# Performance work log

Hardware: AMD Instinct MI355X
Metric: run time of the kernel (lower is better)

Reference implementation:

```python
import jax, jax.numpy as jnp
import numpy as np

N_NODES = 50000
N_EDGES = 800000
N_GRAPHS = 256
F_IN = 112   # num_features
DIM = 32     # hidden dim of 2nd GIN layer
OUT_DIM = 64 # output_dim
BN_EPS = 1e-5


def setup_inputs() -> dict:
    key = jax.random.key(0)
    ks = jax.random.split(key, 20)
    def w(k, shape, s=0.05):
        return jax.random.normal(k, shape, dtype=jnp.float32) * s
    return {
        "x": jax.random.normal(ks[0], (N_NODES, F_IN), dtype=jnp.float32),
        "src": jax.random.randint(ks[1], (N_EDGES,), 0, N_NODES),
        "dst": jax.random.randint(ks[2], (N_EDGES,), 0, N_NODES),
        "batch": jnp.sort(jax.random.randint(ks[3], (N_NODES,), 0, N_GRAPHS)),
        # GIN layer 1 MLP: Linear(112,112) -> ReLU -> Linear(112,112)
        "g1_w1": w(ks[4], (F_IN, F_IN)), "g1_b1": jnp.zeros((F_IN,), jnp.float32),
        "g1_w2": w(ks[5], (F_IN, F_IN)), "g1_b2": jnp.zeros((F_IN,), jnp.float32),
        "bn1_g": jnp.ones((F_IN,), jnp.float32), "bn1_b": jnp.zeros((F_IN,), jnp.float32),
        # GIN layer 2 MLP: Linear(112,32) -> ReLU -> Linear(32,32)
        "g2_w1": w(ks[6], (F_IN, DIM)), "g2_b1": jnp.zeros((DIM,), jnp.float32),
        "g2_w2": w(ks[7], (DIM, DIM)), "g2_b2": jnp.zeros((DIM,), jnp.float32),
        "bn2_g": jnp.ones((DIM,), jnp.float32), "bn2_b": jnp.zeros((DIM,), jnp.float32),
        # graph-level head
        "fcxd_w": w(ks[8], (DIM, OUT_DIM)), "fcxd_b": jnp.zeros((OUT_DIM,), jnp.float32),
        "fc1_w": w(ks[9], (64, 32)), "fc1_b": jnp.zeros((32,), jnp.float32),
        "fc2_w": w(ks[10], (32, 16)), "fc2_b": jnp.zeros((16,), jnp.float32),
        "fc3_w": w(ks[11], (16, 8)), "fc3_b": jnp.zeros((8,), jnp.float32),
        "fc4_w": w(ks[12], (8, 2)), "fc4_b": jnp.zeros((2,), jnp.float32),
        "fc5_w": w(ks[13], (2, 1)), "fc5_b": jnp.zeros((1,), jnp.float32),
    }


def _batchnorm(h, g, b):
    # training-mode BatchNorm1d: batch statistics over node axis
    m = h.mean(axis=0)
    v = h.var(axis=0)
    return (h - m) * jax.lax.rsqrt(v + BN_EPS) * g + b


def reference(x, src, dst, batch,
              g1_w1, g1_b1, g1_w2, g1_b2, bn1_g, bn1_b,
              g2_w1, g2_b1, g2_w2, g2_b2, bn2_g, bn2_b,
              fcxd_w, fcxd_b, fc1_w, fc1_b, fc2_w, fc2_b,
              fc3_w, fc3_b, fc4_w, fc4_b, fc5_w, fc5_b):
    # --- GIN layer 1: agg = sum_{j in N(i)} x_j ; h = MLP(x + agg) (eps=0) ---
    agg = jax.ops.segment_sum(x[src], dst, num_segments=N_NODES)
    h = x + agg
    h = jnp.maximum(h @ g1_w1 + g1_b1, 0.0) @ g1_w2 + g1_b2
    h = jnp.maximum(h, 0.0)                     # F.relu after conv
    h = _batchnorm(h, bn1_g, bn1_b)
    # --- GIN layer 2 ---
    agg = jax.ops.segment_sum(h[src], dst, num_segments=N_NODES)
    h = h + agg
    h = jnp.maximum(h @ g2_w1 + g2_b1, 0.0) @ g2_w2 + g2_b2
    h = jnp.maximum(h, 0.0)
    h = _batchnorm(h, bn2_g, bn2_b)
    # --- global_add_pool over graph ids ---
    pooled = jax.ops.segment_sum(h, batch, num_segments=N_GRAPHS)  # [G, 32]
    z = jnp.maximum(pooled @ fcxd_w + fcxd_b, 0.0)  # dropout = identity (eval)
    # dense head: NO activations between fc1..fc5 in the original code
    z = z @ fc1_w + fc1_b
    z = z @ fc2_w + fc2_b
    z = z @ fc3_w + fc3_b
    z = z @ fc4_w + fc4_b
    z = z @ fc5_w + fc5_b
    return z  # [N_GRAPHS, 1]
```

## Files before the change

### kernel.cpp

```cpp
#include <hip/hip_runtime.h>
#include <hip/hip_fp16.h>

#define N_NODES 50000
#define N_GRAPHS 256
#define N_EDGES 800000
#define F_IN 112
#define DIM 32
#define BN_EPS 1e-5
#define HROW 128
#define CAP 64
#define CB 391
#define CBCAP 2560
#define CHUNK 8192
#define NPART 98
#define GEMM_MB 782
#define WS 40
#define SENT2 0xC350C350u

typedef __attribute__((ext_vector_type(8))) _Float16 half8;
typedef __attribute__((ext_vector_type(4))) float float4v;

__device__ inline unsigned short f2h_u(float f) {
    union { __half h; unsigned short u; } v; v.h = __float2half(f); return v.u;
}
__device__ inline float h2f_u(unsigned short u) {
    union { unsigned short u; __half h; } v; v.u = u; return __half2float(v.h);
}

__device__ inline void acc8(const uint4& u, float* ax) {
    const __half2* h = (const __half2*)&u;
#pragma unroll
    for (int p = 0; p < 4; p++) {
        float2 f = __half22float2(h[p]);
        ax[2 * p] += f.x;
        ax[2 * p + 1] += f.y;
    }
}

__device__ inline void w_split_body(const float* __restrict__ W, int K, int N, int Kpad,
                                    unsigned short* __restrict__ hi_t,
                                    unsigned short* __restrict__ lo_t, int idx) {
    if (idx >= N * Kpad) return;
    int n = idx / Kpad, k = idx - n * Kpad;
    float v = (k < K) ? W[(size_t)k * N + n] : 0.f;
    unsigned short h = f2h_u(v);
    hi_t[idx] = h;
    lo_t[idx] = f2h_u(v - h2f_u(h));
}

#define MB_P  NPART
#define MB_XH (MB_P + 3126)
#define MB_W1 (MB_XH + 14)
#define MB_W2 (MB_W1 + 14)
#define MB_W4 (MB_W2 + 1)
#define MB_GB (MB_W4 + 49)
__global__ __launch_bounds__(1024) void build_kernel(
        const int* __restrict__ src, const int* __restrict__ dst,
        int* __restrict__ gcur,
        int* __restrict__ bucket,
        const float* __restrict__ X, __half* __restrict__ Xh,
        const float* __restrict__ g1_w1, unsigned short* w1h, unsigned short* w1l,
        const float* __restrict__ g1_w2, unsigned short* w2h, unsigned short* w2l,
        const float* __restrict__ g2_w2, unsigned short* w4h, unsigned short* w4l,
        const int* __restrict__ batch, int* __restrict__ goff) {
    int b = blockIdx.x;
    int t = threadIdx.x;
    if (b < MB_P) {
        __shared__ int hist[512];
        __shared__ int lofs[512];
        __shared__ int lcur[512];
        __shared__ int gbase[512];
        __shared__ int staging[CHUNK];
        int base = b * CHUNK;
        int total = min(CHUNK, N_EDGES - base);
        for (int i = t; i < 512; i += 1024) hist[i] = 0;
        __syncthreads();
        int d[8], s[8];
#pragma unroll
        for (int j = 0; j < 8; j++) {
            int i = base + j * 1024 + t;
            if (i < N_EDGES) {
                d[j] = __builtin_nontemporal_load(dst + i);
                s[j] = __builtin_nontemporal_load(src + i);
            } else {
                d[j] = -1;
            }
        }
#pragma unroll
        for (int j = 0; j < 8; j++) {
            if (d[j] >= 0) atomicAdd(&hist[d[j] >> 7], 1);
        }
        __syncthreads();
        if (t < 512) lofs[t] = hist[t];
        __syncthreads();
        for (int o = 1; o < 512; o <<= 1) {
            int add = (t < 512 && t >= o) ? lofs[t - o] : 0;
            __syncthreads();
            if (t < 512) lofs[t] += add;
            __syncthreads();
        }
        if (t < CB) {
            gbase[t] = (hist[t] > 0) ? atomicAdd(&gcur[t], hist[t]) : 0;
        }
        if (t < 512) lcur[t] = lofs[t] - hist[t];
        __syncthreads();
#pragma unroll
        for (int j = 0; j < 8; j++) {
            if (d[j] >= 0) {
                int bb = d[j] >> 7;
                int p = atomicAdd(&lcur[bb], 1);
                staging[p] = (d[j] << 16) | s[j];
            }
        }
        __syncthreads();
        for (int p = t; p < total; p += 1024) {
            int e = staging[p];
            int bb = ((unsigned)e >> 16) >> 7;
            int ls = lofs[bb] - hist[bb];
            int di = gbase[bb] + (p - ls);
            if (di < CBCAP) bucket[(size_t)bb * CBCAP + di] = e;
        }
    } else if (b < MB_XH) {
        int idx = (b - MB_P) * 1024 + t;
        if (idx >= (N_NODES + 1) * (HROW / 2)) return;
        int row = idx >> 6, c2 = idx & 63;
        int col = c2 * 2;
        float2 v = make_float2(0.f, 0.f);
        if (row < N_NODES && col < F_IN) v = *(const float2*)(X + (size_t)row * F_IN + col);
        ((__half2*)Xh)[idx] = __floats2half2_rn(v.x, v.y);
    } else if (b < MB_W1) {
        w_split_body(g1_w1, F_IN, F_IN, 128, w1h, w1l, (b - MB_XH) * 1024 + t);
    } else if (b < MB_W2) {
        w_split_body(g1_w2, F_IN, F_IN, 128, w2h, w2l, (b - MB_W1) * 1024 + t);
    } else if (b < MB_W4) {
        w_split_body(g2_w2, DIM, DIM, 32, w4h, w4l, (b - MB_W2) * 1024 + t);
    } else {
        int i = (b - MB_W4) * 1024 + t;
        if (i >= N_NODES) return;
        int cur = batch[i];
        int prev = (i == 0) ? -1 : batch[i - 1];
        for (int g = prev + 1; g <= cur; g++) goff[g] = i;
        if (i == N_NODES - 1) {
            for (int g = cur + 1; g <= N_GRAPHS; g++) goff[g] = N_NODES;
        }
    }
}

__global__ __launch_bounds__(1024, 8) void gin1_fused(const float* __restrict__ X,
        const __half* __restrict__ Xh,
        const int* __restrict__ gcur,
        const int* __restrict__ bucket,
        const unsigned short* __restrict__ W1h, const unsigned short* __restrict__ W1l,
        const float* __restrict__ b1,
        const unsigned short* __restrict__ W2h, const unsigned short* __restrict__ W2l,
        const float* __restrict__ b2,
        __half* __restrict__ Ch, float* __restrict__ pbuf, int M) {
    constexpr int N = 112, Kpad = 128, TS = 136, AS = 136;
    __shared__ __align__(16) unsigned short Afull[64 * AS];
    __shared__ __align__(16) unsigned short T1[64 * TS];
    __shared__ __align__(16) unsigned short Wh[N * WS];
    __shared__ __align__(16) unsigned short Wl[N * WS];
    __shared__ __align__(16) unsigned short bins[64][CAP];
    __shared__ int lcur[64];
    float* sls = (float*)Afull;
    int t = threadIdx.x;
    int lane = t & 63, wid = t >> 6;
    int r0 = blockIdx.x * 64;
    int m = lane & 15, quad = lane >> 4;
    int rg = wid & 3, ng = wid >> 2;
    int nt0 = ng, nt1 = ng + 4;
    bool has1 = (nt1 < 7);

    for (int i = t; i < 64 * CAP / 2; i += 1024) ((unsigned int*)bins)[i] = SENT2;
    if (t < 64) lcur[t] = 0;

    for (int idx = t; idx < N * 8; idx += 1024) {
        int n = idx >> 3, w = idx & 7;
        int gsrc = n * (Kpad / 4) + w;
        ((uint2*)&Wh[n * WS])[w] = ((const uint2*)W1h)[gsrc];
        ((uint2*)&Wl[n * WS])[w] = ((const uint2*)W1l)[gsrc];
    }
    __syncthreads();

    {
        int cb = blockIdx.x >> 1, half = blockIdx.x & 1;
        int count = min(gcur[cb], CBCAP);
        for (int i = t; i < count; i += 1024) {
            int e = bucket[(size_t)cb * CBCAP + i];
            int l = ((unsigned)e >> 16) & 127;
            if ((l >> 6) == half) {
                int c = atomicAdd(&lcur[l & 63], 1);
                if (c < CAP) bins[l & 63][c] = (unsigned short)(e & 0xFFFF);
            }
        }
    }
    __syncthreads();

    int fl = lane & 15, eg = lane >> 4;
#pragma unroll 1
    for (int i = 0; i < 4; i++) {
        int row = wid * 4 + i;
        int grow = r0 + row;
        int deg = min(lcur[row], CAP);
        float ax[8] = {0.f, 0.f, 0.f, 0.f, 0.f, 0.f, 0.f, 0.f};
        const unsigned short* pl = bins[row];
        int nb = (deg + 3) >> 2;
#pragma unroll 1
        for (int b = 0; b < nb; b += 4) {
            int s0 = pl[(b + 0) * 4 + eg];
            int s1 = pl[(b + 1) * 4 + eg];
            int s2 = pl[(b + 2) * 4 + eg];
            int s3 = pl[(b + 3) * 4 + eg];
            uint4 u0 = *(const uint4*)(Xh + (size_t)s0 * HROW + fl * 8);
            uint4 u1 = *(const uint4*)(Xh + (size_t)s1 * HROW + fl * 8);
            uint4 u2 = *(const uint4*)(Xh + (size_t)s2 * HROW + fl * 8);
            uint4 u3 = *(const uint4*)(Xh + (size_t)s3 * HROW + fl * 8);
            acc8(u0, ax); acc8(u1, ax); acc8(u2, ax); acc8(u3, ax);
        }
#pragma unroll
        for (int p = 0; p < 8; p++) {
            ax[p] += __shfl_xor(ax[p], 16);
            ax[p] += __shfl_xor(ax[p], 32);
        }
        if (eg == 0) {
            if (grow < M && fl < 14) {
                float4 sa = *(const float4*)(X + (size_t)grow * F_IN + fl * 8);
                float4 sb = *(const float4*)(X + (size_t)grow * F_IN + fl * 8 + 4);
                ax[0] += sa.x; ax[1] += sa.y; ax[2] += sa.z; ax[3] += sa.w;
                ax[4] += sb.x; ax[5] += sb.y; ax[6] += sb.z; ax[7] += sb.w;
            }
            uint4 o;
            __half2* oh = (__half2*)&o;
#pragma unroll
            for (int p = 0; p < 4; p++) oh[p] = __floats2half2_rn(ax[2 * p], ax[2 * p + 1]);
            *(uint4*)&Afull[row * AS + fl * 8] = o;
        }
    }
    {
        int i = t;
        T1[(i >> 4) * TS + 112 + (i & 15)] = 0;
    }

    float4v acc0 = {0.f, 0.f, 0.f, 0.f}, acc1 = {0.f, 0.f, 0.f, 0.f};

    for (int c = 0; c < 4; c++) {
        int kc = c * 32;
        if (c > 0) {
            for (int idx = t; idx < N * 8; idx += 1024) {
                int n = idx >> 3, w = idx & 7;
                int gsrc = n * (Kpad / 4) + (kc >> 2) + w;
                ((uint2*)&Wh[n * WS])[w] = ((const uint2*)W1h)[gsrc];
                ((uint2*)&Wl[n * WS])[w] = ((const uint2*)W1l)[gsrc];
            }
        }
        __syncthreads();
        half8 a = *(const half8*)&Afull[(rg * 16 + m) * AS + kc + quad * 8];
        {
            half8 bh = *(const half8*)&Wh[(nt0 * 16 + m) * WS + quad * 8];
            half8 bl = *(const half8*)&Wl[(nt0 * 16 + m) * WS + quad * 8];
            acc0 = __builtin_amdgcn_mfma_f32_16x16x32_f16(a, bh, acc0, 0, 0, 0);
            acc0 = __builtin_amdgcn_mfma_f32_16x16x32_f16(a, bl, acc0, 0, 0, 0);
        }
        if (has1) {
            half8 bh = *(const half8*)&Wh[(nt1 * 16 + m) * WS + quad * 8];
            half8 bl = *(const half8*)&Wl[(nt1 * 16 + m) * WS + quad * 8];
            acc1 = __builtin_amdgcn_mfma_f32_16x16x32_f16(a, bh, acc1, 0, 0, 0);
            acc1 = __builtin_amdgcn_mfma_f32_16x16x32_f16(a, bl, acc1, 0, 0, 0);
        }
        __syncthreads();
    }

    {
        int col = nt0 * 16 + m;
        float bb = b1[col];
#pragma unroll
        for (int r = 0; r < 4; r++)
            T1[(rg * 16 + quad * 4 + r) * TS + col] = f2h_u(fmaxf(acc0[r] + bb, 0.f));
        acc0 = (float4v){0.f, 0.f, 0.f, 0.f};
    }
    if (has1) {
        int col = nt1 * 16 + m;
        float bb = b1[col];
#pragma unroll
        for (int r = 0; r < 4; r++)
            T1[(rg * 16 + quad * 4 + r) * TS + col] = f2h_u(fmaxf(acc1[r] + bb, 0.f));
        acc1 = (float4v){0.f, 0.f, 0.f, 0.f};
    }
    __syncthreads();

    for (int c = 0; c < 4; c++) {
        int kc = c * 32;
        for (int idx = t; idx < N * 8; idx += 1024) {
            int n = idx >> 3, w = idx & 7;
            int gsrc = n * (Kpad / 4) + (kc >> 2) + w;
            ((uint2*)&Wh[n * WS])[w] = ((const uint2*)W2h)[gsrc];
            ((uint2*)&Wl[n * WS])[w] = ((const uint2*)W2l)[gsrc];
        }
        __syncthreads();
        half8 a = *(const half8*)&T1[(rg * 16 + m) * TS + kc + quad * 8];
        {
            half8 bh = *(const half8*)&Wh[(nt0 * 16 + m) * WS + quad * 8];
            half8 bl = *(const half8*)&Wl[(nt0 * 16 + m) * WS + quad * 8];
            acc0 = __builtin_amdgcn_mfma_f32_16x16x32_f16(a, bh, acc0, 0, 0, 0);
            acc0 = __builtin_amdgcn_mfma_f32_16x16x32_f16(a, bl, acc0, 0, 0, 0);
        }
        if (has1) {
            half8 bh = *(const half8*)&Wh[(nt1 * 16 + m) * WS + quad * 8];
            half8 bl = *(const half8*)&Wl[(nt1 * 16 + m) * WS + quad * 8];
            acc1 = __builtin_amdgcn_mfma_f32_16x16x32_f16(a, bh, acc1, 0, 0, 0);
            acc1 = __builtin_amdgcn_mfma_f32_16x16x32_f16(a, bl, acc1, 0, 0, 0);
        }
        __syncthreads();
    }

    float st_s0 = 0.f, st_q0 = 0.f, st_s1 = 0.f, st_q1 = 0.f;
    {
        int col = nt0 * 16 + m;
        float bb = b2[col];
#pragma unroll
        for (int r = 0; r < 4; r++) {
            int row = r0 + rg * 16 + quad * 4 + r;
            float v = fmaxf(acc0[r] + bb, 0.f);
            if (row < M) {
                Ch[(size_t)row * HROW + col] = __float2half(v);
                st_s0 += v;
                st_q0 += v * v;
            }
        }
    }
    if (has1) {
        int col = nt1 * 16 + m;
        float bb = b2[col];
#pragma unroll
        for (int r = 0; r < 4; r++) {
            int row = r0 + rg * 16 + quad * 4 + r;
            float v = fmaxf(acc1[r] + bb, 0.f);
            if (row < M) {
                Ch[(size_t)row * HROW + col] = __float2half(v);
                st_s1 += v;
                st_q1 += v * v;
            }
        }
    }
    if (t < 128) {
        int row = r0 + (t >> 1), o = (t & 1) * 8;
        if (row < M) *(uint4*)((unsigned short*)Ch + (size_t)row * HROW + 112 + o) = make_uint4(0, 0, 0, 0);
    }
    st_s0 += __shfl_xor(st_s0, 16); st_s0 += __shfl_xor(st_s0, 32);
    st_q0 += __shfl_xor(st_q0, 16); st_q0 += __shfl_xor(st_q0, 32);
    st_s1 += __shfl_xor(st_s1, 16); st_s1 += __shfl_xor(st_s1, 32);
    st_q1 += __shfl_xor(st_q1, 16); st_q1 += __shfl_xor(st_q1, 32);
    if (quad == 0) {
        sls[rg * 2 * N + nt0 * 16 + m] = st_s0;
        sls[rg * 2 * N + N + nt0 * 16 + m] = st_q0;
        if (has1) {
            sls[rg * 2 * N + nt1 * 16 + m] = st_s1;
            sls[rg * 2 * N + N + nt1 * 16 + m] = st_q1;
        }
    }
    __syncthreads();
    if (t < 2 * N) {
        pbuf[(size_t)blockIdx.x * 2 * N + t] = sls[0 * 2 * N + t] + sls[1 * 2 * N + t] +
                                               sls[2 * 2 * N + t] + sls[3 * 2 * N + t];
    }
}

__global__ __launch_bounds__(256) void bn1_w3(const float* __restrict__ pbuf,
                                              const float* __restrict__ gg,
                                              const float* __restrict__ bb,
                                              const float* __restrict__ W,
                                              unsigned short* __restrict__ w3h,
                                              unsigned short* __restrict__ w3l,
                                              float* __restrict__ c0,
                                              __half* __restrict__ ysent, int M) {
    __shared__ double red[256];
    __shared__ float sv[2];
    int j = blockIdx.x;
    int t = threadIdx.x;
    if (j == 0 && t >= 64 && t < 96) ysent[t - 64] = __float2half(0.f);
    double sum = 0.0, sq = 0.0;
    for (int i = t; i < GEMM_MB; i += 256) {
        sum += (double)pbuf[(size_t)i * 2 * F_IN + j];
        sq  += (double)pbuf[(size_t)i * 2 * F_IN + F_IN + j];
    }
    red[t] = sum;
    __syncthreads();
    for (int o = 128; o > 0; o >>= 1) { if (t < o) red[t] += red[t + o]; __syncthreads(); }
    double total_sum = red[0];
    __syncthreads();
    red[t] = sq;
    __syncthreads();
    for (int o = 128; o > 0; o >>= 1) { if (t < o) red[t] += red[t + o]; __syncthreads(); }
    if (t == 0) {
        double mean = total_sum / M;
        double var = red[0] / M - mean * mean;
        double sc = (double)gg[j] / sqrt(var + BN_EPS);
        sv[0] = (float)sc;
        sv[1] = (float)((double)bb[j] - mean * sc);
    }
    __syncthreads();
    if (t < DIM) {
        float w = W[(size_t)j * DIM + t];
        float v = sv[0] * w;
        unsigned short h = f2h_u(v);
        w3h[t * 128 + j] = h;
        w3l[t * 128 + j] = f2h_u(v - h2f_u(h));
        atomicAdd(&c0[t], sv[1] * w);
    }
}

template <int NT, int KC, int ASG, int CHS>
__global__ __launch_bounds__(256) void gemm_mfma_h(const unsigned short* __restrict__ A,
                                                   const unsigned short* __restrict__ Whi,
                                                   const unsigned short* __restrict__ Wlo,
                                                   __half* __restrict__ Ch, int M) {
    constexpr int N = NT * 16;
    constexpr int Kpad = KC * 32;
    __shared__ __align__(16) unsigned short Ah[64 * WS];
    __shared__ __align__(16) unsigned short Wh[N * WS];
    __shared__ __align__(16) unsigned short Wl[N * WS];
    int t = threadIdx.x;
    int lane = t & 63, wid = t >> 6;
    int r0 = blockIdx.x * 64;
    int m = lane & 15, quad = lane >> 4;

    float4v acc[NT];
#pragma unroll
    for (int nt = 0; nt < NT; nt++) acc[nt] = (float4v){0.f, 0.f, 0.f, 0.f};

    for (int c = 0; c < KC; c++) {
        int kc = c * 32;
        {
            int row = t >> 2, seg = t & 3;
            int grow = r0 + row;
            uint4 v = make_uint4(0, 0, 0, 0);
            if (grow < M) v = *(const uint4*)(A + (size_t)grow * ASG + kc + seg * 8);
            *(uint4*)&Ah[row * WS + seg * 8] = v;
        }
        for (int idx = t; idx < N * 8; idx += 256) {
            int n = idx >> 3, w = idx & 7;
            int gsrc = n * (Kpad / 4) + (kc >> 2) + w;
            ((uint2*)&Wh[n * WS])[w] = ((const uint2*)Whi)[gsrc];
            ((uint2*)&Wl[n * WS])[w] = ((const uint2*)Wlo)[gsrc];
        }
        __syncthreads();
        half8 a = *(const half8*)&Ah[(wid * 16 + m) * WS + quad * 8];
#pragma unroll
        for (int nt = 0; nt < NT; nt++) {
            half8 b_h = *(const half8*)&Wh[(nt * 16 + m) * WS + quad * 8];
            half8 b_l = *(const half8*)&Wl[(nt * 16 + m) * WS + quad * 8];
            acc[nt] = __builtin_amdgcn_mfma_f32_16x16x32_f16(a, b_h, acc[nt], 0, 0, 0);
            acc[nt] = __builtin_amdgcn_mfma_f32_16x16x32_f16(a, b_l, acc[nt], 0, 0, 0);
        }
        __syncthreads();
    }
#pragma unroll
    for (int nt = 0; nt < NT; nt++) {
        int col = nt * 16 + m;
#pragma unroll
        for (int r = 0; r < 4; r++) {
            int row = r0 + wid * 16 + quad * 4 + r;
            if (row < M) Ch[(size_t)row * CHS + col] = __float2half(acc[nt][r]);
        }
    }
}

__global__ __launch_bounds__(512, 8) void gin2_fused(const __half* __restrict__ Y,
        const int* __restrict__ gcur,
        const int* __restrict__ bucket,
        const float* __restrict__ c0, const float* __restrict__ cb1,
        const unsigned short* __restrict__ W4h, const unsigned short* __restrict__ W4l,
        const float* __restrict__ bias,
        float* __restrict__ C, float* __restrict__ pbuf, int M) {
    constexpr int N = 32;
    __shared__ __align__(16) unsigned short As[64 * WS];
    __shared__ __align__(16) unsigned short Wh[N * WS];
    __shared__ __align__(16) unsigned short Wl[N * WS];
    __shared__ __align__(16) unsigned short bins[64][CAP];
    __shared__ int lcur[64];
    __shared__ float sls[4][2 * N];
    int t = threadIdx.x;
    int lane = t & 63, wid = t >> 6;
    int r0 = blockIdx.x * 64;
    int m = lane & 15, quad = lane >> 4;
    int rg = wid & 3, nt = wid >> 2;

    for (int i = t; i < 64 * CAP / 2; i += 512) ((unsigned int*)bins)[i] = SENT2;
    if (t < 64) lcur[t] = 0;

    for (int idx = t; idx < N * 8; idx += 512) {
        int n = idx >> 3, w = idx & 7;
        int gsrc = n * 8 + w;
        ((uint2*)&Wh[n * WS])[w] = ((const uint2*)W4h)[gsrc];
        ((uint2*)&Wl[n * WS])[w] = ((const uint2*)W4l)[gsrc];
    }
    __syncthreads();

    {
        int cb = blockIdx.x >> 1, half = blockIdx.x & 1;
        int count = min(gcur[cb], CBCAP);
        for (int i = t; i < count; i += 512) {
            int e = bucket[(size_t)cb * CBCAP + i];
            int l = ((unsigned)e >> 16) & 127;
            if ((l >> 6) == half) {
                int c = atomicAdd(&lcur[l & 63], 1);
                if (c < CAP) bins[l & 63][c] = (unsigned short)(e & 0xFFFF);
            }
        }
    }
    __syncthreads();

    int seg = lane & 3, eg = lane >> 2;
#pragma unroll 1
    for (int i = 0; i < 8; i++) {
        int row = wid * 8 + i;
        int grow = r0 + row;
        int deg = min(lcur[row], CAP);
        float ax[8] = {0.f, 0.f, 0.f, 0.f, 0.f, 0.f, 0.f, 0.f};
        if (grow < M) {
            const unsigned short* pl = bins[row];
            int s[4];
#pragma unroll
            for (int j = 0; j < 4; j++) s[j] = pl[j * 16 + eg];
            uint4 u[4];
#pragma unroll
            for (int j = 0; j < 4; j++) u[j] = *(const uint4*)(Y + (size_t)s[j] * DIM + seg * 8);
#pragma unroll
            for (int j = 0; j < 4; j++) acc8(u[j], ax);
        }
#pragma unroll
        for (int p = 0; p < 8; p++) {
            ax[p] += __shfl_xor(ax[p], 4);
            ax[p] += __shfl_xor(ax[p], 8);
            ax[p] += __shfl_xor(ax[p], 16);
            ax[p] += __shfl_xor(ax[p], 32);
        }
        if (eg == 0) {
            uint4 o = make_uint4(0, 0, 0, 0);
            if (grow < M) {
                uint4 sv = *(const uint4*)(Y + (size_t)grow * DIM + seg * 8);
                float deg1 = (float)(deg + 1);
                const __half2* sh = (const __half2*)&sv;
                __half2* oh = (__half2*)&o;
#pragma unroll
                for (int p = 0; p < 4; p++) {
                    float2 sf = __half22float2(sh[p]);
                    int f0 = seg * 8 + 2 * p;
                    float zx = fmaxf(sf.x + ax[2 * p] + deg1 * c0[f0] + cb1[f0], 0.f);
                    float zy = fmaxf(sf.y + ax[2 * p + 1] + deg1 * c0[f0 + 1] + cb1[f0 + 1], 0.f);
                    oh[p] = __floats2half2_rn(zx, zy);
                }
            }
            *(uint4*)&As[row * WS + seg * 8] = o;
        }
    }
    __syncthreads();

    float4v acc = {0.f, 0.f, 0.f, 0.f};
    half8 a = *(const half8*)&As[(rg * 16 + m) * WS + quad * 8];
    half8 bh = *(const half8*)&Wh[(nt * 16 + m) * WS + quad * 8];
    half8 bl = *(const half8*)&Wl[(nt * 16 + m) * WS + quad * 8];
    acc = __builtin_amdgcn_mfma_f32_16x16x32_f16(a, bh, acc, 0, 0, 0);
    acc = __builtin_amdgcn_mfma_f32_16x16x32_f16(a, bl, acc, 0, 0, 0);

    int col = nt * 16 + m;
    float b = bias[col];
    float s_loc = 0.f, q_loc = 0.f;
#pragma unroll
    for (int r = 0; r < 4; r++) {
        int row = r0 + rg * 16 + quad * 4 + r;
        float v = fmaxf(acc[r] + b, 0.f);
        if (row < M) {
            C[(size_t)row * N + col] = v;
            s_loc += v;
            q_loc += v * v;
        }
    }
    s_loc += __shfl_xor(s_loc, 16); s_loc += __shfl_xor(s_loc, 32);
    q_loc += __shfl_xor(q_loc, 16); q_loc += __shfl_xor(q_loc, 32);
    if (quad == 0) {
        sls[rg][col] = s_loc;
        sls[rg][N + col] = q_loc;
    }
    __syncthreads();
    if (t < 2 * N) {
        pbuf[(size_t)blockIdx.x * 2 * N + t] = sls[0][t] + sls[1][t] + sls[2][t] + sls[3][t];
    }
}

template <int F, int BLOCKS>
__global__ __launch_bounds__(256) void bn_finalize_par(const float* __restrict__ pbuf,
                                                       const float* __restrict__ g,
                                                       const float* __restrict__ b,
                                                       float* __restrict__ s,
                                                       float* __restrict__ tt, int M) {
    __shared__ double red[256];
    int j = blockIdx.x;
    int t = threadIdx.x;
    double sum = 0.0, sq = 0.0;
    for (int i = t; i < BLOCKS; i += 256) {
        sum += (double)pbuf[(size_t)i * 2 * F + j];
        sq  += (double)pbuf[(size_t)i * 2 * F + F + j];
    }
    red[t] = sum;
    __syncthreads();
    for (int o = 128; o > 0; o >>= 1) { if (t < o) red[t] += red[t + o]; __syncthreads(); }
    double total_sum = red[0];
    __syncthreads();
    red[t] = sq;
    __syncthreads();
    for (int o = 128; o > 0; o >>= 1) { if (t < o) red[t] += red[t + o]; __syncthreads(); }
    if (t == 0) {
        double mean = total_sum / M;
        double var = red[0] / M - mean * mean;
        double sc = (double)g[j] / sqrt(var + BN_EPS);
        s[j] = (float)sc;
        tt[j] = (float)((double)b[j] - mean * sc);
    }
}

__global__ __launch_bounds__(256) void pool_head(const float* __restrict__ H2, const int* __restrict__ goff,
                                                 const float* __restrict__ s2, const float* __restrict__ t2,
                                                 const float* __restrict__ fcxd_w, const float* __restrict__ fcxd_b,
                                                 const float* __restrict__ fc1_w, const float* __restrict__ fc1_b,
                                                 const float* __restrict__ fc2_w, const float* __restrict__ fc2_b,
                                                 const float* __restrict__ fc3_w, const float* __restrict__ fc3_b,
                                                 const float* __restrict__ fc4_w, const float* __restrict__ fc4_b,
                                                 const float* __restrict__ fc5_w, const float* __restrict__ fc5_b,
                                                 float* __restrict__ out) {
    __shared__ float red[256];
    __shared__ float p[64];
    __shared__ float z[64];
    int g = blockIdx.x, t = threadIdx.x;
    int r0 = goff[g], r1 = goff[g + 1];
    int cnt = r1 - r0;
    int j = t & 31, rr = t >> 5;
    float a = 0.f;
    for (int r = r0 + rr; r < r1; r += 8) a += H2[(size_t)r * DIM + j];
    red[t] = a;
    __syncthreads();
    if (t < 32) {
        float ssum = 0.f;
        for (int q = 0; q < 8; q++) ssum += red[q * 32 + j];
        p[j] = s2[j] * ssum + (float)cnt * t2[j];
    }
    __syncthreads();
    if (t < 64) {
        float acc = fcxd_b[t];
        for (int i = 0; i < 32; i++) acc += p[i] * fcxd_w[i * 64 + t];
        z[t] = fmaxf(acc, 0.f);
    }
    __syncthreads();
    if (t < 32) {
        float acc = fc1_b[t];
        for (int i = 0; i < 64; i++) acc += z[i] * fc1_w[i * 32 + t];
        p[t] = acc;
    }
    __syncthreads();
    if (t < 16) {
        float acc = fc2_b[t];
        for (int i = 0; i < 32; i++) acc += p[i] * fc2_w[i * 16 + t];
        z[t] = acc;
    }
    __syncthreads();
    if (t < 8) {
        float acc = fc3_b[t];
        for (int i = 0; i < 16; i++) acc += z[i] * fc3_w[i * 8 + t];
        p[t] = acc;
    }
    __syncthreads();
    if (t < 2) {
        float acc = fc4_b[t];
        for (int i = 0; i < 8; i++) acc += p[i] * fc4_w[i * 2 + t];
        z[t] = acc;
    }
    __syncthreads();
    if (t == 0) {
        out[g] = z[0] * fc5_w[0] + z[1] * fc5_w[1] + fc5_b[0];
    }
}

extern "C" void kernel_launch(void* const* d_in, const int* in_sizes, int n_in,
                              void* d_out, int out_size, void* d_ws, size_t ws_size,
                              hipStream_t stream) {
    const float* x     = (const float*)d_in[0];
    const int*   src   = (const int*)d_in[1];
    const int*   dst   = (const int*)d_in[2];
    const int*   batch = (const int*)d_in[3];
    const float* g1_w1 = (const float*)d_in[4];
    const float* g1_b1 = (const float*)d_in[5];
    const float* g1_w2 = (const float*)d_in[6];
    const float* g1_b2 = (const float*)d_in[7];
    const float* bn1_g = (const float*)d_in[8];
    const float* bn1_b = (const float*)d_in[9];
    const float* g2_w1 = (const float*)d_in[10];
    const float* g2_b1 = (const float*)d_in[11];
    const float* g2_w2 = (const float*)d_in[12];
    const float* g2_b2 = (const float*)d_in[13];
    const float* bn2_g = (const float*)d_in[14];
    const float* bn2_b = (const float*)d_in[15];
    const float* fcxd_w = (const float*)d_in[16];
    const float* fcxd_b = (const float*)d_in[17];
    const float* fc1_w = (const float*)d_in[18];
    const float* fc1_b = (const float*)d_in[19];
    const float* fc2_w = (const float*)d_in[20];
    const float* fc2_b = (const float*)d_in[21];
    const float* fc3_w = (const float*)d_in[22];
    const float* fc3_b = (const float*)d_in[23];
    const float* fc4_w = (const float*)d_in[24];
    const float* fc4_b = (const float*)d_in[25];
    const float* fc5_w = (const float*)d_in[26];
    const float* fc5_b = (const float*)d_in[27];
    float* out = (float*)d_out;
    char* ws = (char*)d_ws;

    size_t off = 0;
    auto take = [&](size_t bytes) { size_t o = off; off += (bytes + 255) & ~(size_t)255; return o; };
    int* gcur      = (int*)(ws + take((size_t)CB * 4));
    float* c0      = (float*)(ws + take(DIM * 4));
    unsigned short* w3h = (unsigned short*)(ws + take((size_t)DIM * 128 * 2));
    unsigned short* w3l = (unsigned short*)(ws + take((size_t)DIM * 128 * 2));
    size_t zero_bytes = off;
    int* bucket    = (int*)(ws + take((size_t)CB * CBCAP * 4));
    int* goff      = (int*)(ws + take((size_t)(N_GRAPHS + 4) * 4));
    float* s2      = (float*)(ws + take(DIM * 4));
    float* t2      = (float*)(ws + take(DIM * 4));
    float* pb1     = (float*)(ws + take((size_t)GEMM_MB * 2 * F_IN * 4));
    float* pb2     = (float*)(ws + take((size_t)GEMM_MB * 2 * DIM * 4));
    unsigned short* w1h = (unsigned short*)(ws + take((size_t)F_IN * 128 * 2));
    unsigned short* w1l = (unsigned short*)(ws + take((size_t)F_IN * 128 * 2));
    unsigned short* w2h = (unsigned short*)(ws + take((size_t)F_IN * 128 * 2));
    unsigned short* w2l = (unsigned short*)(ws + take((size_t)F_IN * 128 * 2));
    unsigned short* w4h = (unsigned short*)(ws + take((size_t)DIM * 32 * 2));
    unsigned short* w4l = (unsigned short*)(ws + take((size_t)DIM * 32 * 2));
    __half* x_half = (__half*)(ws + take((size_t)(N_NODES + 1) * HROW * 2));
    __half* h1h    = (__half*)(ws + take((size_t)N_NODES * HROW * 2));
    __half* y_half = (__half*)(ws + take((size_t)(N_NODES + 1) * DIM * 2));
    float* bufS2   = (float*)(ws + take((size_t)N_NODES * DIM * 4));
    (void)ws_size; (void)in_sizes; (void)n_in; (void)out_size;

    hipMemsetAsync(ws, 0, zero_bytes, stream);

    build_kernel<<<MB_GB, 1024, 0, stream>>>(src, dst, gcur, bucket,
                                             x, x_half,
                                             g1_w1, w1h, w1l, g1_w2, w2h, w2l, g2_w2, w4h, w4l,
                                             batch, goff);

    gin1_fused<<<GEMM_MB, 1024, 0, stream>>>(x, x_half, gcur, bucket,
                                             w1h, w1l, g1_b1, w2h, w2l, g1_b2,
                                             h1h, pb1, N_NODES);
    bn1_w3<<<F_IN, 256, 0, stream>>>(pb1, bn1_g, bn1_b, g2_w1, w3h, w3l, c0,
                                     y_half + (size_t)N_NODES * DIM, N_NODES);

    gemm_mfma_h<2, 4, HROW, DIM><<<GEMM_MB, 256, 0, stream>>>(
        (const unsigned short*)h1h, w3h, w3l, y_half, N_NODES);
    gin2_fused<<<GEMM_MB, 512, 0, stream>>>(y_half, gcur, bucket, c0, g2_b1,
                                            w4h, w4l, g2_b2, bufS2, pb2, N_NODES);
    bn_finalize_par<DIM, GEMM_MB><<<DIM, 256, 0, stream>>>(pb2, bn2_g, bn2_b, s2, t2, N_NODES);

    pool_head<<<N_GRAPHS, 256, 0, stream>>>(bufS2, goff, s2, t2,
                                            fcxd_w, fcxd_b, fc1_w, fc1_b, fc2_w, fc2_b,
                                            fc3_w, fc3_b, fc4_w, fc4_b, fc5_w, fc5_b, out);
}
```

Before: 243.0 us.

## Halve gin1_fused block size and reuse A-tile LDS for the hidden activations

gin1_fused now runs with 512 threads instead of 1024. Each wave gathers 8 rows instead of 4, and in each MFMA step it covers up to 4 output column tiles, reusing one A fragment across them. The separate T1 shared buffer for the first MLP's hidden output is removed; that output is written back in place into Afull after the first GEMM finishes. This cuts LDS use per block and should let more blocks stay resident per CU, with the aim of better latency hiding in the gather and GEMM phases. The cost is more serialized work per wave, a longer per-wave gather loop, and more accumulator registers.

```diff
diff --git a/kernel.cpp b/kernel.cpp
--- a/kernel.cpp
+++ b/kernel.cpp
@@ -146,7 +146,7 @@
     }
 }
 
-__global__ __launch_bounds__(1024, 8) void gin1_fused(const float* __restrict__ X,
+__global__ __launch_bounds__(512, 6) void gin1_fused(const float* __restrict__ X,
         const __half* __restrict__ Xh,
         const int* __restrict__ gcur,
         const int* __restrict__ bucket,
@@ -155,9 +155,8 @@
         const unsigned short* __restrict__ W2h, const unsigned short* __restrict__ W2l,
         const float* __restrict__ b2,
         __half* __restrict__ Ch, float* __restrict__ pbuf, int M) {
-    constexpr int N = 112, Kpad = 128, TS = 136, AS = 136;
+    constexpr int N = 112, Kpad = 128, AS = 136;
     __shared__ __align__(16) unsigned short Afull[64 * AS];
-    __shared__ __align__(16) unsigned short T1[64 * TS];
     __shared__ __align__(16) unsigned short Wh[N * WS];
     __shared__ __align__(16) unsigned short Wl[N * WS];
     __shared__ __align__(16) unsigned short bins[64][CAP];
@@ -167,14 +166,12 @@
     int lane = t & 63, wid = t >> 6;
     int r0 = blockIdx.x * 64;
     int m = lane & 15, quad = lane >> 4;
-    int rg = wid & 3, ng = wid >> 2;
-    int nt0 = ng, nt1 = ng + 4;
-    bool has1 = (nt1 < 7);
-
-    for (int i = t; i < 64 * CAP / 2; i += 1024) ((unsigned int*)bins)[i] = SENT2;
+    int rg = wid & 3, ng2 = wid >> 2;
+
+    for (int i = t; i < 64 * CAP / 2; i += 512) ((unsigned int*)bins)[i] = SENT2;
     if (t < 64) lcur[t] = 0;
 
-    for (int idx = t; idx < N * 8; idx += 1024) {
+    for (int idx = t; idx < N * 8; idx += 512) {
         int n = idx >> 3, w = idx & 7;
         int gsrc = n * (Kpad / 4) + w;
         ((uint2*)&Wh[n * WS])[w] = ((const uint2*)W1h)[gsrc];
@@ -185,7 +182,7 @@
     {
         int cb = blockIdx.x >> 1, half = blockIdx.x & 1;
         int count = min(gcur[cb], CBCAP);
-        for (int i = t; i < count; i += 1024) {
+        for (int i = t; i < count; i += 512) {
             int e = bucket[(size_t)cb * CBCAP + i];
             int l = ((unsigned)e >> 16) & 127;
             if ((l >> 6) == half) {
@@ -198,8 +195,8 @@
 
     int fl = lane & 15, eg = lane >> 4;
 #pragma unroll 1
-    for (int i = 0; i < 4; i++) {
-        int row = wid * 4 + i;
+    for (int i = 0; i < 8; i++) {
+        int row = wid * 8 + i;
         int grow = r0 + row;
         int deg = min(lcur[row], CAP);
         float ax[8] = {0.f, 0.f, 0.f, 0.f, 0.f, 0.f, 0.f, 0.f};
@@ -236,17 +233,15 @@
             *(uint4*)&Afull[row * AS + fl * 8] = o;
         }
     }
-    {
-        int i = t;
-        T1[(i >> 4) * TS + 112 + (i & 15)] = 0;
-    }
-
-    float4v acc0 = {0.f, 0.f, 0.f, 0.f}, acc1 = {0.f, 0.f, 0.f, 0.f};
+
+    float4v acc[4];
+#pragma unroll
+    for (int k = 0; k < 4; k++) acc[k] = (float4v){0.f, 0.f, 0.f, 0.f};
 
     for (int c = 0; c < 4; c++) {
         int kc = c * 32;
         if (c > 0) {
-            for (int idx = t; idx < N * 8; idx += 1024) {
+            for (int idx = t; idx < N * 8; idx += 512) {
                 int n = idx >> 3, w = idx & 7;
                 int gsrc = n * (Kpad / 4) + (kc >> 2) + w;
                 ((uint2*)&Wh[n * WS])[w] = ((const uint2*)W1h)[gsrc];
@@ -255,90 +250,71 @@
         }
         __syncthreads();
         half8 a = *(const half8*)&Afull[(rg * 16 + m) * AS + kc + quad * 8];
-        {
-            half8 bh = *(const half8*)&Wh[(nt0 * 16 + m) * WS + quad * 8];
-            half8 bl = *(const half8*)&Wl[(nt0 * 16 + m) * WS + quad * 8];
-            acc0 = __builtin_amdgcn_mfma_f32_16x16x32_f16(a, bh, acc0, 0, 0, 0);
-            acc0 = __builtin_amdgcn_mfma_f32_16x16x32_f16(a, bl, acc0, 0, 0, 0);
-        }
-        if (has1) {
-            half8 bh = *(const half8*)&Wh[(nt1 * 16 + m) * WS + quad * 8];
-            half8 bl = *(const half8*)&Wl[(nt1 * 16 + m) * WS + quad * 8];
-            acc1 = __builtin_amdgcn_mfma_f32_16x16x32_f16(a, bh, acc1, 0, 0, 0);
-            acc1 = __builtin_amdgcn_mfma_f32_16x16x32_f16(a, bl, acc1, 0, 0, 0);
-        }
-        __syncthreads();
-    }
-
-    {
-        int col = nt0 * 16 + m;
-        float bb = b1[col];
-#pragma unroll
-        for (int r = 0; r < 4; r++)
-            T1[(rg * 16 + quad * 4 + r) * TS + col] = f2h_u(fmaxf(acc0[r] + bb, 0.f));
-        acc0 = (float4v){0.f, 0.f, 0.f, 0.f};
-    }
-    if (has1) {
-        int col = nt1 * 16 + m;
-        float bb = b1[col];
-#pragma unroll
-        for (int r = 0; r < 4; r++)
-            T1[(rg * 16 + quad * 4 + r) * TS + col] = f2h_u(fmaxf(acc1[r] + bb, 0.f));
-        acc1 = (float4v){0.f, 0.f, 0.f, 0.f};
-    }
-    __syncthreads();
+#pragma unroll
+        for (int k = 0; k < 4; k++) {
+            int nt = ng2 + 2 * k;
+            if (nt < 7) {
+                half8 bh = *(const half8*)&Wh[(nt * 16 + m) * WS + quad * 8];
+                half8 bl = *(const half8*)&Wl[(nt * 16 + m) * WS + quad * 8];
+                acc[k] = __builtin_amdgcn_mfma_f32_16x16x32_f16(a, bh, acc[k], 0, 0, 0);
+                acc[k] = __builtin_amdgcn_mfma_f32_16x16x32_f16(a, bl, acc[k], 0, 0, 0);
+            }
+        }
+        __syncthreads();
+    }
+
+#pragma unroll
+    for (int k = 0; k < 4; k++) {
+        int nt = ng2 + 2 * k;
+        if (nt < 7) {
+            int col = nt * 16 + m;
+            float bb = b1[col];
+#pragma unroll
+            for (int r = 0; r < 4; r++)
+                Afull[(rg * 16 + quad * 4 + r) * AS + col] = f2h_u(fmaxf(acc[k][r] + bb, 0.f));
+            acc[k] = (float4v){0.f, 0.f, 0.f, 0.f};
+        }
+    }
 
     for (int c = 0; c < 4; c++) {
         int kc = c * 32;
-        for (int idx = t; idx < N * 8; idx += 1024) {
+        for (int idx = t; idx < N * 8; idx += 512) {
             int n = idx >> 3, w = idx & 7;
             int gsrc = n * (Kpad / 4) + (kc >> 2) + w;
             ((uint2*)&Wh[n * WS])[w] = ((const uint2*)W2h)[gsrc];
             ((uint2*)&Wl[n * WS])[w] = ((const uint2*)W2l)[gsrc];
         }
         __syncthreads();
-        half8 a = *(const half8*)&T1[(rg * 16 + m) * TS + kc + quad * 8];
-        {
-            half8 bh = *(const half8*)&Wh[(nt0 * 16 + m) * WS + quad * 8];
-            half8 bl = *(const half8*)&Wl[(nt0 * 16 + m) * WS + quad * 8];
-            acc0 = __builtin_amdgcn_mfma_f32_16x16x32_f16(a, bh, acc0, 0, 0, 0);
-            acc0 = __builtin_amdgcn_mfma_f32_16x16x32_f16(a, bl, acc0, 0, 0, 0);
-        }
-        if (has1) {
-            half8 bh = *(const half8*)&Wh[(nt1 * 16 + m) * WS + quad * 8];
-            half8 bl = *(const half8*)&Wl[(nt1 * 16 + m) * WS + quad * 8];
-            acc1 = __builtin_amdgcn_mfma_f32_16x16x32_f16(a, bh, acc1, 0, 0, 0);
-            acc1 = __builtin_amdgcn_mfma_f32_16x16x32_f16(a, bl, acc1, 0, 0, 0);
-        }
-        __syncthreads();
-    }
-
-    float st_s0 = 0.f, st_q0 = 0.f, st_s1 = 0.f, st_q1 = 0.f;
-    {
-        int col = nt0 * 16 + m;
-        float bb = b2[col];
-#pragma unroll
-        for (int r = 0; r < 4; r++) {
-            int row = r0 + rg * 16 + quad * 4 + r;
-            float v = fmaxf(acc0[r] + bb, 0.f);
-            if (row < M) {
-                Ch[(size_t)row * HROW + col] = __float2half(v);
-                st_s0 += v;
-                st_q0 += v * v;
-            }
-        }
-    }
-    if (has1) {
-        int col = nt1 * 16 + m;
-        float bb = b2[col];
-#pragma unroll
-        for (int r = 0; r < 4; r++) {
-            int row = r0 + rg * 16 + quad * 4 + r;
-            float v = fmaxf(acc1[r] + bb, 0.f);
-            if (row < M) {
-                Ch[(size_t)row * HROW + col] = __float2half(v);
-                st_s1 += v;
-                st_q1 += v * v;
+        half8 a = *(const half8*)&Afull[(rg * 16 + m) * AS + kc + quad * 8];
+#pragma unroll
+        for (int k = 0; k < 4; k++) {
+            int nt = ng2 + 2 * k;
+            if (nt < 7) {
+                half8 bh = *(const half8*)&Wh[(nt * 16 + m) * WS + quad * 8];
+                half8 bl = *(const half8*)&Wl[(nt * 16 + m) * WS + quad * 8];
+                acc[k] = __builtin_amdgcn_mfma_f32_16x16x32_f16(a, bh, acc[k], 0, 0, 0);
+                acc[k] = __builtin_amdgcn_mfma_f32_16x16x32_f16(a, bl, acc[k], 0, 0, 0);
+            }
+        }
+        __syncthreads();
+    }
+
+    float st_s[4] = {0.f, 0.f, 0.f, 0.f}, st_q[4] = {0.f, 0.f, 0.f, 0.f};
+#pragma unroll
+    for (int k = 0; k < 4; k++) {
+        int nt = ng2 + 2 * k;
+        if (nt < 7) {
+            int col = nt * 16 + m;
+            float bb = b2[col];
+#pragma unroll
+            for (int r = 0; r < 4; r++) {
+                int row = r0 + rg * 16 + quad * 4 + r;
+                float v = fmaxf(acc[k][r] + bb, 0.f);
+                if (row < M) {
+                    Ch[(size_t)row * HROW + col] = __float2half(v);
+                    st_s[k] += v;
+                    st_q[k] += v * v;
+                }
             }
         }
     }
@@ -346,22 +322,21 @@
         int row = r0 + (t >> 1), o = (t & 1) * 8;
         if (row < M) *(uint4*)((unsigned short*)Ch + (size_t)row * HROW + 112 + o) = make_uint4(0, 0, 0, 0);
     }
-    st_s0 += __shfl_xor(st_s0, 16); st_s0 += __shfl_xor(st_s0, 32);
-    st_q0 += __shfl_xor(st_q0, 16); st_q0 += __shfl_xor(st_q0, 32);
-    st_s1 += __shfl_xor(st_s1, 16); st_s1 += __shfl_xor(st_s1, 32);
-    st_q1 += __shfl_xor(st_q1, 16); st_q1 += __shfl_xor(st_q1, 32);
-    if (quad == 0) {
-        sls[rg * 2 * N + nt0 * 16 + m] = st_s0;
-        sls[rg * 2 * N + N + nt0 * 16 + m] = st_q0;
-        if (has1) {
-            sls[rg * 2 * N + nt1 * 16 + m] = st_s1;
-            sls[rg * 2 * N + N + nt1 * 16 + m] = st_q1;
-        }
-    }
-    __syncthreads();
-    if (t < 2 * N) {
-        pbuf[(size_t)blockIdx.x * 2 * N + t] = sls[0 * 2 * N + t] + sls[1 * 2 * N + t] +
-                                               sls[2 * 2 * N + t] + sls[3 * 2 * N + t];
+#pragma unroll
+    for (int k = 0; k < 4; k++) {
+        int nt = ng2 + 2 * k;
+        float s = st_s[k], q = st_q[k];
+        s += __shfl_xor(s, 16); s += __shfl_xor(s, 32);
+        q += __shfl_xor(q, 16); q += __shfl_xor(q, 32);
+        if (nt < 7 && quad == 0) {
+            sls[rg * 2 * N + nt * 16 + m] = s;
+            sls[rg * 2 * N + N + nt * 16 + m] = q;
+        }
+    }
+    __syncthreads();
+    for (int j = t; j < 2 * N; j += 512) {
+        pbuf[(size_t)blockIdx.x * 2 * N + j] = sls[0 * 2 * N + j] + sls[1 * 2 * N + j] +
+                                               sls[2 * 2 * N + j] + sls[3 * 2 * N + j];
     }
 }
 
@@ -746,9 +721,9 @@
                                              g1_w1, w1h, w1l, g1_w2, w2h, w2l, g2_w2, w4h, w4l,
                                              batch, goff);
 
-    gin1_fused<<<GEMM_MB, 1024, 0, stream>>>(x, x_half, gcur, bucket,
-                                             w1h, w1l, g1_b1, w2h, w2l, g1_b2,
-                                             h1h, pb1, N_NODES);
+    gin1_fused<<<GEMM_MB, 512, 0, stream>>>(x, x_half, gcur, bucket,
+                                            w1h, w1l, g1_b1, w2h, w2l, g1_b2,
+                                            h1h, pb1, N_NODES);
     bn1_w3<<<F_IN, 256, 0, stream>>>(pb1, bn1_g, bn1_b, g2_w1, w3h, w3l, c0,
                                      y_half + (size_t)N_NODES * DIM, N_NODES);
 
```

New measurement: 252.6 us. 3.9% more time.
